# Kernel tuning notes

Measured on AMD Instinct MI355X. Metric: run time of the kernel, lower is better.

Reference implementation:

```python
import jax, jax.numpy as jnp
import numpy as np

B, DIM, H, W = 8, 128, 128, 128
QK, MLP, HEADS, NT, GS = 128, 256, 4, 8, 128


def _ln(x, w, b):
    m = jnp.mean(x, -1, keepdims=True)
    v = jnp.mean((x - m) ** 2, -1, keepdims=True)
    return (x - m) * jax.lax.rsqrt(v + 1e-5) * w + b


def _norml2(x):
    n = jnp.sqrt(jnp.sum(x * x, -1, keepdims=True))
    return x / jnp.maximum(n, 1e-12)


def setup_inputs() -> dict:
    key = jax.random.key(0)
    ks = jax.random.split(key, 12)
    s = 0.02
    f32 = jnp.float32
    return {
        'x': jax.random.normal(ks[0], (B, DIM, H, W), f32),
        'means': jax.random.normal(ks[1], (NT, DIM), f32),
        'ln1_w': jnp.ones((DIM,), f32), 'ln1_b': jnp.zeros((DIM,), f32),
        'wq': jax.random.normal(ks[2], (QK, DIM), f32) * s,
        'wk': jax.random.normal(ks[3], (QK, DIM), f32) * s,
        'wv': jax.random.normal(ks[4], (DIM, DIM), f32) * s,
        'wproj': jax.random.normal(ks[5], (DIM, DIM), f32) * s,
        'irca_wk': jax.random.normal(ks[6], (QK, DIM), f32) * s,
        'irca_wv': jax.random.normal(ks[7], (DIM, DIM), f32) * s,
        'conv1x1_w': jax.random.normal(ks[8], (DIM, DIM), f32) * s,
        'ln2_w': jnp.ones((DIM,), f32), 'ln2_b': jnp.zeros((DIM,), f32),
        'fc1_w': jax.random.normal(ks[9], (MLP, DIM), f32) * s,
        'fc1_b': jnp.zeros((MLP,), f32),
        'dw_w': jax.random.normal(ks[10], (MLP, 1, 5, 5), f32) * s,
        'dw_b': jnp.zeros((MLP,), f32),
        'fc2_w': jax.random.normal(ks[11], (DIM, MLP), f32) * s,
        'fc2_b': jnp.zeros((DIM,), f32),
    }


def reference(x, means, ln1_w, ln1_b, wq, wk, wv, wproj, irca_wk, irca_wv,
              conv1x1_w, ln2_w, ln2_b, fc1_w, fc1_b, dw_w, dw_b, fc2_w, fc2_b):
    Bx, C, Hh, Ww = x.shape
    N = Hh * Ww
    xt = x.reshape(Bx, C, N).transpose(0, 2, 1)          # b n c
    residual = xt
    xn = _ln(xt, ln1_w, ln1_b)
    m = jax.lax.stop_gradient(means)                      # eval: means buffer, detached
    # IRCA (eval path): global K/V from cluster means
    dq, dv = QK // HEADS, C // HEADS
    kg = (m @ irca_wk.T).reshape(NT, HEADS, dq).transpose(1, 0, 2)  # h nt dq
    vg = (m @ irca_wv.T).reshape(NT, HEADS, dv).transpose(1, 0, 2)  # h nt dv
    # cluster assignment -> token reordering (no grad)
    scores = jnp.einsum('bic,jc->bij', _norml2(xn), _norml2(m))
    buckets = jnp.argmax(scores, axis=-1)
    idx = jnp.argsort(buckets, axis=-1)                   # [B,N] permutation
    # IASA
    q = xn @ wq.T
    k = xn @ wk.T
    v = xn @ wv.T
    take = lambda t: jnp.take_along_axis(t, idx[:, :, None], axis=1)
    q, k, v = take(q), take(k), take(v)
    gs = min(N, GS)
    ng = (N + gs - 1) // gs
    pad_n = ng * gs - N
    qp = jnp.concatenate([q, jnp.flip(q[:, N - pad_n:N], axis=1)], axis=1)
    qp = qp.reshape(Bx, ng, gs, HEADS, dq).transpose(0, 1, 3, 2, 4)  # b g h gs dq

    def window(t, d):
        tp = jnp.concatenate([t, jnp.flip(t[:, N - pad_n - gs:N], axis=1)], axis=1)
        blk = tp.reshape(Bx, ng + 1, gs, HEADS, d)
        win = jnp.concatenate([blk[:, :-1], blk[:, 1:]], axis=2)     # b g 2gs h d
        return win.transpose(0, 1, 3, 2, 4)

    kp = window(k, dq)
    vp = window(v, dv)
    scale = 1.0 / np.sqrt(dq)
    a1 = jax.nn.softmax(jnp.einsum('bghqd,bghkd->bghqk', qp, kp) * scale, axis=-1)
    out1 = jnp.einsum('bghqk,bghkd->bghqd', a1, vp)
    a2 = jax.nn.softmax(jnp.einsum('bghqd,hkd->bghqk', qp, kg) * scale, axis=-1)
    out2 = jnp.einsum('bghqk,hkd->bghqd', a2, vg)
    out = (out1 + out2).transpose(0, 1, 3, 2, 4).reshape(Bx, ng * gs, C)[:, :N]
    inv = jnp.argsort(idx, axis=-1)                       # scatter-back = inverse perm
    out = jnp.take_along_axis(out, inv[:, :, None], axis=1)
    out = out @ wproj.T
    yimg = out.transpose(0, 2, 1).reshape(Bx, C, Hh, Ww)
    yimg = jnp.einsum('oc,bchw->bohw', conv1x1_w, yimg)
    x2 = residual + yimg.reshape(Bx, C, N).transpose(0, 2, 1)
    # ConvFFN with PreNorm
    xm = _ln(x2, ln2_w, ln2_b)
    h1 = jax.nn.gelu(xm @ fc1_w.T + fc1_b, approximate=False)
    himg = h1.transpose(0, 2, 1).reshape(Bx, MLP, Hh, Ww)
    dwc = jax.lax.conv_general_dilated(himg, dw_w, (1, 1), 'SAME',
                                       feature_group_count=MLP,
                                       dimension_numbers=('NCHW', 'OIHW', 'NCHW'))
    dwc = jax.nn.gelu(dwc + dw_b.reshape(1, MLP, 1, 1), approximate=False)
    h1 = h1 + dwc.reshape(Bx, MLP, N).transpose(0, 2, 1)
    x3 = x2 + (h1 @ fc2_w.T + fc2_b)
    return x3.transpose(0, 2, 1).reshape(Bx, C, Hh, Ww)
```

## Files before the change

kernel.cpp:

```cpp
#include <hip/hip_runtime.h>
#include <math.h>

typedef unsigned short u16;
typedef unsigned int u32;
typedef __attribute__((ext_vector_type(8))) short bf16x8;
typedef __attribute__((ext_vector_type(4))) float f32x4;

constexpr int BB   = 8;
constexpr int DIMC = 128;
constexpr int HH   = 128;
constexpr int WW   = 128;
constexpr int NTOK = HH * WW;
constexpr int QKD  = 128;
constexpr int MLPD = 256;
constexpr int NTm  = 8;
constexpr int GSZ  = 128;
constexpr int NGRP = NTOK / GSZ;
constexpr size_t BIG = 16777216;

__device__ __forceinline__ float gelu_f(float v) {
    return 0.5f * v * (1.0f + erff(v * 0.70710678118654752440f));
}
__device__ __forceinline__ float b2f(u16 u) {
    return __uint_as_float(((u32)u) << 16);
}
__device__ __forceinline__ u16 f2b(float f) {
    u32 x = __float_as_uint(f);
    return (u16)((x + 0x7fffu + ((x >> 16) & 1u)) >> 16);
}
__device__ __forceinline__ float ulo(u32 u) { return __uint_as_float(u << 16); }
__device__ __forceinline__ float uhi(u32 u) { return __uint_as_float(u & 0xffff0000u); }

__global__ __launch_bounds__(128) void k_prep(const float* __restrict__ means,
        const float* __restrict__ iwk, const float* __restrict__ iwv,
        float* __restrict__ mhat, u16* __restrict__ kgbb, u16* __restrict__ vgtb) {
    __shared__ float sm[DIMC];
    __shared__ float inv_s;
    int tt = blockIdx.x;
    int t = threadIdx.x;
    sm[t] = means[tt * DIMC + t];
    __syncthreads();
    if (t == 0) {
        float s = 0.f;
        for (int c = 0; c < DIMC; c++) s += sm[c] * sm[c];
        inv_s = 1.f / fmaxf(sqrtf(s), 1e-12f);
    }
    __syncthreads();
    mhat[tt * DIMC + t] = sm[t] * inv_s;
    float sk = 0.f, sv = 0.f;
    #pragma unroll 8
    for (int c = 0; c < DIMC; c++) {
        sk = fmaf(sm[c], iwk[t * DIMC + c], sk);
        sv = fmaf(sm[c], iwv[t * DIMC + c], sv);
    }
    kgbb[tt * DIMC + t] = f2b(sk);
    vgtb[(t >> 5) * 256 + (t & 31) * 8 + tt] = f2b(sv);
}

__global__ __launch_bounds__(256) void k_cvtall(const float* __restrict__ wq,
        const float* __restrict__ wk, const float* __restrict__ wv,
        const float* __restrict__ fc1, const float* __restrict__ fc2,
        u16* __restrict__ wqkv, u16* __restrict__ fc1b, u16* __restrict__ fc2b) {
    int i = blockIdx.x * 256 + threadIdx.x;
    if (i < 49152) {
        const float* s = (i < 16384) ? wq : (i < 32768 ? wk : wv);
        wqkv[i] = f2b(s[i & 16383]);
    } else if (i < 81920) {
        fc1b[i - 49152] = f2b(fc1[i - 49152]);
    } else if (i < 114688) {
        fc2b[i - 81920] = f2b(fc2[i - 81920]);
    }
}

__global__ __launch_bounds__(256) void k_fuse(const float* __restrict__ c1,
        const float* __restrict__ wp, u16* __restrict__ wf) {
    __shared__ float wpS[DIMC * DIMC];
    int t = threadIdx.x;
    for (int i = t; i < DIMC * DIMC; i += 256) wpS[i] = wp[i];
    __syncthreads();
    int o = blockIdx.x * 2 + (t >> 7);
    int c = t & 127;
    float s = 0.f;
    #pragma unroll 8
    for (int m = 0; m < DIMC; m++) s = fmaf(c1[o * DIMC + m], wpS[m * DIMC + c], s);
    wf[o * DIMC + c] = f2b(s);
}

__global__ __launch_bounds__(64) void k_ln1(const float* __restrict__ x,
        const float* __restrict__ lw, const float* __restrict__ lb,
        const float* __restrict__ mhat, u16* __restrict__ xn, int* __restrict__ bucket) {
    __shared__ float smh[NTm * DIMC];
    int chunk = blockIdx.x;
    int b = chunk >> 8;
    int n = ((chunk & 255) << 6) + threadIdx.x;
    for (int i = threadIdx.x; i < NTm * DIMC; i += 64) smh[i] = mhat[i];
    __syncthreads();
    const float* xb = x + (size_t)b * DIMC * NTOK + n;
    float xv[DIMC];
    float sum = 0.f, sq = 0.f;
    #pragma unroll
    for (int c = 0; c < DIMC; c++) {
        float v = xb[(size_t)c * NTOK];
        xv[c] = v;
        sum += v; sq += v * v;
    }
    float mean = sum * (1.0f / DIMC);
    float var = sq * (1.0f / DIMC) - mean * mean;
    float rstd = rsqrtf(var + 1e-5f);
    float sc[NTm];
    #pragma unroll
    for (int j = 0; j < NTm; j++) sc[j] = 0.f;
    u16* xnr = xn + ((size_t)b * NTOK + n) * DIMC;
    #pragma unroll
    for (int c = 0; c < DIMC; c++) {
        float v = (xv[c] - mean) * rstd * lw[c] + lb[c];
        xnr[c] = f2b(v);
        #pragma unroll
        for (int j = 0; j < NTm; j++) sc[j] = fmaf(v, smh[j * DIMC + c], sc[j]);
    }
    int best = 0; float bv = sc[0];
    #pragma unroll
    for (int j = 1; j < NTm; j++) if (sc[j] > bv) { bv = sc[j]; best = j; }
    bucket[b * NTOK + n] = best;
}

__global__ __launch_bounds__(64) void k_count(const int* __restrict__ bucket, int* __restrict__ cnt) {
    int chunk = blockIdx.x;
    int bk = bucket[(chunk << 6) + threadIdx.x];
    #pragma unroll
    for (int j = 0; j < NTm; j++) {
        unsigned long long m = __ballot(bk == j);
        if (threadIdx.x == 0) cnt[chunk * NTm + j] = (int)__popcll(m);
    }
}

__global__ __launch_bounds__(64) void k_scan(const int* __restrict__ cnt, int* __restrict__ base) {
    __shared__ int sc[256 * NTm];
    __shared__ int bb[NTm], tot[NTm];
    int b = blockIdx.x, t = threadIdx.x;
    for (int i = t; i < 256 * NTm; i += 64) sc[i] = cnt[b * 256 * NTm + i];
    __syncthreads();
    if (t < NTm) {
        int run = 0;
        for (int c = 0; c < 256; c++) {
            int v = sc[c * NTm + t];
            sc[c * NTm + t] = run;
            run += v;
        }
        tot[t] = run;
    }
    __syncthreads();
    if (t == 0) {
        int a = 0;
        for (int j = 0; j < NTm; j++) { bb[j] = a; a += tot[j]; }
    }
    __syncthreads();
    for (int i = t; i < 256 * NTm; i += 64) base[b * 256 * NTm + i] = sc[i] + bb[i & 7];
}

__global__ __launch_bounds__(64) void k_place(const int* __restrict__ bucket,
        const int* __restrict__ base, int* __restrict__ gidx) {
    int chunk = blockIdx.x;
    int lane = threadIdx.x;
    int nf = (chunk << 6) + lane;
    int bk = bucket[nf];
    unsigned long long lower = (1ull << lane) - 1ull;
    int rank = 0;
    #pragma unroll
    for (int j = 0; j < NTm; j++) {
        unsigned long long m = __ballot(bk == j);
        if (bk == j) rank = (int)__popcll(m & lower);
    }
    int b = nf >> 14;
    int pos = base[chunk * NTm + bk] + rank;
    gidx[b * NTOK + pos] = nf & (NTOK - 1);
}

__global__ __launch_bounds__(256) void k_inv(const int* __restrict__ gidx, u16* __restrict__ iinv) {
    int i = blockIdx.x * 256 + threadIdx.x;
    int b = i >> 14;
    iinv[((size_t)b << 14) + gidx[i]] = (u16)(i & (NTOK - 1));
}

template<int KDIM, int NOUT, int GATHER, int AIMG, int BIASF, int GELUF, int RES, int STIMG, int CBF, int LN2F>
__global__ __launch_bounds__(256) void g_mfma(const u16* __restrict__ A, const u16* __restrict__ W,
        const float* __restrict__ bias, const void* __restrict__ resid,
        const int* __restrict__ gidx, void* __restrict__ Cout, float ascale,
        const float* __restrict__ lnw, const float* __restrict__ lnb, void* __restrict__ Cout2) {
    __shared__ u16 As[128 * 40];
    __shared__ u16 Ws[128 * 40];
    const int b = blockIdx.z;
    const int m0 = blockIdx.x * 128;
    const int n0 = blockIdx.y * 128;
    const int t = threadIdx.x;
    const int lane = t & 63;
    const int wave = t >> 6;
    const int wm = (wave & 1) * 64;
    const int wn = (wave >> 1) * 64;
    const int srow = t >> 2;
    const int sko = (t & 3) * 8;
    const u16* pA0 = nullptr; const u16* pA1 = nullptr;
    if (!AIMG) {
        int ra0 = m0 + srow, ra1 = m0 + 64 + srow;
        if (GATHER == 1) {
            ra0 = gidx[b * NTOK + ra0];
            ra1 = gidx[b * NTOK + ra1];
        } else if (GATHER == 2) {
            const u16* gi = (const u16*)gidx;
            ra0 = gi[b * NTOK + ra0];
            ra1 = gi[b * NTOK + ra1];
        }
        pA0 = A + ((size_t)b * NTOK + ra0) * KDIM + sko;
        pA1 = A + ((size_t)b * NTOK + ra1) * KDIM + sko;
    }
    const u16* pW0 = W + (size_t)(n0 + srow) * KDIM + sko;
    const u16* pW1 = W + (size_t)(n0 + 64 + srow) * KDIM + sko;

    f32x4 acc[4][4];
    #pragma unroll
    for (int i = 0; i < 4; i++)
        #pragma unroll
        for (int j = 0; j < 4; j++) acc[i][j] = (f32x4){0.f, 0.f, 0.f, 0.f};

    for (int k0 = 0; k0 < KDIM; k0 += 32) {
        uint4 a0, a1, w0, w1;
        u16 e[16];
        if (!AIMG) {
            a0 = *(const uint4*)(pA0 + k0);
            a1 = *(const uint4*)(pA1 + k0);
        } else {
            const int kk2 = t & 31;
            const int tg = t >> 5;
            const u16* src = A + ((size_t)b * KDIM + k0 + kk2) * NTOK + m0 + tg * 16;
            *(uint4*)&e[0] = *(const uint4*)src;
            *(uint4*)&e[8] = *(const uint4*)(src + 8);
        }
        w0 = *(const uint4*)(pW0 + k0);
        w1 = *(const uint4*)(pW1 + k0);
        __syncthreads();
        if (!AIMG) {
            *(uint4*)&As[srow * 40 + sko] = a0;
            *(uint4*)&As[(64 + srow) * 40 + sko] = a1;
        } else {
            const int kk2 = t & 31;
            const int tg = t >> 5;
            #pragma unroll
            for (int j = 0; j < 16; j++) As[(tg * 16 + j) * 40 + kk2] = e[j];
        }
        *(uint4*)&Ws[srow * 40 + sko] = w0;
        *(uint4*)&Ws[(64 + srow) * 40 + sko] = w1;
        __syncthreads();
        bf16x8 af[4], bfv[4];
        #pragma unroll
        for (int i = 0; i < 4; i++)
            af[i] = *(bf16x8*)&As[(wm + i * 16 + (lane & 15)) * 40 + (lane >> 4) * 8];
        #pragma unroll
        for (int j = 0; j < 4; j++)
            bfv[j] = *(bf16x8*)&Ws[(wn + j * 16 + (lane & 15)) * 40 + (lane >> 4) * 8];
        #pragma unroll
        for (int i = 0; i < 4; i++)
            #pragma unroll
            for (int j = 0; j < 4; j++)
                acc[i][j] = __builtin_amdgcn_mfma_f32_16x16x32_bf16(af[i], bfv[j], acc[i][j], 0, 0, 0);
    }

    const int c2 = lane & 15, gq2 = lane >> 4;
    int colj[4];
    #pragma unroll
    for (int j = 0; j < 4; j++) colj[j] = n0 + wn + j * 16 + c2;

    if (LN2F) {
        #pragma unroll
        for (int i = 0; i < 4; i++) {
            int rbase = m0 + wm + i * 16 + gq2 * 4;
            #pragma unroll
            for (int j = 0; j < 4; j++) {
                const float* rf = (const float*)resid;
                float4 rr = *(const float4*)&rf[((size_t)b * NOUT + colj[j]) * NTOK + rbase];
                acc[i][j][0] += rr.x; acc[i][j][1] += rr.y;
                acc[i][j][2] += rr.z; acc[i][j][3] += rr.w;
            }
        }
        __syncthreads();
        float* ps = (float*)&As[0];
        const int h = wn >> 6;
        float mean_[4][4], rstd_[4][4];
        #pragma unroll
        for (int i = 0; i < 4; i++)
            #pragma unroll
            for (int r = 0; r < 4; r++) {
                float s = 0.f, q = 0.f;
                #pragma unroll
                for (int j = 0; j < 4; j++) { float tv = acc[i][j][r]; s += tv; q += tv * tv; }
                s += __shfl_xor(s, 1, 64); q += __shfl_xor(q, 1, 64);
                s += __shfl_xor(s, 2, 64); q += __shfl_xor(q, 2, 64);
                s += __shfl_xor(s, 4, 64); q += __shfl_xor(q, 4, 64);
                s += __shfl_xor(s, 8, 64); q += __shfl_xor(q, 8, 64);
                if (c2 == 0) {
                    int rl = wm + i * 16 + gq2 * 4 + r;
                    ps[(h * 128 + rl) * 2 + 0] = s;
                    ps[(h * 128 + rl) * 2 + 1] = q;
                }
            }
        __syncthreads();
        #pragma unroll
        for (int i = 0; i < 4; i++)
            #pragma unroll
            for (int r = 0; r < 4; r++) {
                int rl = wm + i * 16 + gq2 * 4 + r;
                float s = ps[rl * 2 + 0] + ps[(128 + rl) * 2 + 0];
                float q = ps[rl * 2 + 1] + ps[(128 + rl) * 2 + 1];
                float mn = s * (1.0f / 128.0f);
                float vr = q * (1.0f / 128.0f) - mn * mn;
                mean_[i][r] = mn;
                rstd_[i][r] = rsqrtf(vr + 1e-5f);
            }
        float lwj[4], lbj[4];
        #pragma unroll
        for (int j = 0; j < 4; j++) { lwj[j] = lnw[colj[j]]; lbj[j] = lnb[colj[j]]; }
        u16* xo = (u16*)Cout;
        u16* mo = (u16*)Cout2;
        #pragma unroll
        for (int i = 0; i < 4; i++) {
            int rbase = m0 + wm + i * 16 + gq2 * 4;
            #pragma unroll
            for (int j = 0; j < 4; j++)
                #pragma unroll
                for (int r = 0; r < 4; r++) {
                    float tv = acc[i][j][r];
                    size_t off = ((size_t)b * NTOK + rbase + r) * NOUT + colj[j];
                    xo[off] = f2b(tv);
                    mo[off] = f2b((tv - mean_[i][r]) * rstd_[i][r] * lwj[j] + lbj[j]);
                }
        }
        return;
    }

    const float smul = (blockIdx.y == 0) ? ascale : 1.0f;
    float bj[4];
    #pragma unroll
    for (int j = 0; j < 4; j++) bj[j] = BIASF ? bias[colj[j]] : 0.f;
    #pragma unroll
    for (int i = 0; i < 4; i++) {
        int rbase = m0 + wm + i * 16 + gq2 * 4;
        #pragma unroll
        for (int j = 0; j < 4; j++) {
            f32x4 v = acc[i][j];
            v[0] *= smul; v[1] *= smul; v[2] *= smul; v[3] *= smul;
            if (BIASF) { v[0] += bj[j]; v[1] += bj[j]; v[2] += bj[j]; v[3] += bj[j]; }
            if (GELUF) { v[0] = gelu_f(v[0]); v[1] = gelu_f(v[1]); v[2] = gelu_f(v[2]); v[3] = gelu_f(v[3]); }
            if (RES == 1) {
                const float* rf = (const float*)resid;
                float4 rr = *(const float4*)&rf[((size_t)b * NOUT + colj[j]) * NTOK + rbase];
                v[0] += rr.x; v[1] += rr.y; v[2] += rr.z; v[3] += rr.w;
            } else if (RES == 3) {
                const u16* rb = (const u16*)resid;
                #pragma unroll
                for (int r = 0; r < 4; r++)
                    v[r] += b2f(rb[((size_t)b * NTOK + rbase + r) * NOUT + colj[j]]);
            }
            if (STIMG) {
                size_t off = ((size_t)b * NOUT + colj[j]) * NTOK + rbase;
                if (CBF) {
                    ushort4 o;
                    o.x = f2b(v[0]); o.y = f2b(v[1]); o.z = f2b(v[2]); o.w = f2b(v[3]);
                    *(ushort4*)((u16*)Cout + off) = o;
                } else {
                    *(float4*)((float*)Cout + off) = make_float4(v[0], v[1], v[2], v[3]);
                }
            } else {
                if (CBF) {
                    #pragma unroll
                    for (int r = 0; r < 4; r++)
                        ((u16*)Cout)[((size_t)b * NTOK + rbase + r) * NOUT + colj[j]] = f2b(v[r]);
                } else {
                    #pragma unroll
                    for (int r = 0; r < 4; r++)
                        ((float*)Cout)[((size_t)b * NTOK + rbase + r) * NOUT + colj[j]] = v[r];
                }
            }
        }
    }
}

__global__ __launch_bounds__(256, 3) void k_attn(const u16* __restrict__ qkv,
        const u16* __restrict__ kgbb, const u16* __restrict__ vgtb,
        u16* __restrict__ outp) {
    __shared__ u16 VT[2][32][264];
    __shared__ u16 Pb[4][64][40];
    const int g = blockIdx.x, hp = blockIdx.y, b = blockIdx.z;
    const int t = threadIdx.x;
    const int wave = t >> 6, lane = t & 63;
    const int c = lane & 15, gq = lane >> 4;
    const int lh = wave & 1, head = hp * 2 + lh, qh = wave >> 1;
    const size_t brow = (size_t)b * NTOK;

    {
        int key = t;
        int pos = (key < GSZ) ? g * GSZ + key
                : (g == NGRP - 1 ? NTOK - 1 - (key - GSZ) : g * GSZ + key);
        const u16* vp = qkv + (brow + pos) * 384 + 256 + hp * 64;
        #pragma unroll
        for (int i = 0; i < 8; i++) {
            uint4 v = *(const uint4*)(vp + i * 8);
            u16 e[8];
            *(uint4*)e = v;
            #pragma unroll
            for (int j = 0; j < 8; j++) {
                int d = i * 8 + j;
                VT[d >> 5][d & 31][key] = e[j];
            }
        }
        if (t < 64) {
            int l2 = t >> 5, dv = t & 31;
            uint4 v = *(const uint4*)(vgtb + ((size_t)(hp * 2 + l2) * 32 + dv) * 8);
            *(uint4*)&VT[l2][dv][256] = v;
        }
    }

    const int q0 = g * GSZ + qh * 64;
    bf16x8 qf[4];
    #pragma unroll
    for (int nq = 0; nq < 4; nq++)
        qf[nq] = *(const bf16x8*)(qkv + (brow + q0 + nq * 16 + c) * 384 + head * 32 + gq * 8);

    const u16* kbp = qkv + brow * 384 + 128 + head * 32 + gq * 8;
    bf16x8 kfa[8][2];
    #pragma unroll
    for (int s = 0; s < 8; s++)
        #pragma unroll
        for (int mk = 0; mk < 2; mk++) {
            int kl = s * 32 + mk * 16 + c;
            int pos = (kl < GSZ) ? g * GSZ + kl
                    : (g == NGRP - 1 ? NTOK - 1 - (kl - GSZ) : g * GSZ + kl);
            kfa[s][mk] = *(const bf16x8*)(kbp + (size_t)pos * 384);
        }
    bf16x8 kgf = *(const bf16x8*)(kgbb + (c & 7) * 128 + head * 32 + gq * 8);

    __syncthreads();

    f32x4 acc[4][2];
    #pragma unroll
    for (int i = 0; i < 4; i++)
        #pragma unroll
        for (int j = 0; j < 2; j++) acc[i][j] = (f32x4){0.f, 0.f, 0.f, 0.f};
    float lsum[4] = {0.f, 0.f, 0.f, 0.f};

    for (int s = 0; s < 8; s++) {
        #pragma unroll
        for (int mk = 0; mk < 2; mk++) {
            #pragma unroll
            for (int nq = 0; nq < 4; nq++) {
                f32x4 st = __builtin_amdgcn_mfma_f32_16x16x32_bf16(kfa[s][mk], qf[nq],
                        (f32x4){0.f, 0.f, 0.f, 0.f}, 0, 0, 0);
                float p0 = __expf(st[0]), p1 = __expf(st[1]);
                float p2 = __expf(st[2]), p3 = __expf(st[3]);
                lsum[nq] += (p0 + p1) + (p2 + p3);
                u32 r0, r1;
                asm("v_cvt_pk_bf16_f32 %0, %1, %2" : "=v"(r0) : "v"(p0), "v"(p1));
                asm("v_cvt_pk_bf16_f32 %0, %1, %2" : "=v"(r1) : "v"(p2), "v"(p3));
                *(uint2*)&Pb[wave][nq * 16 + c][mk * 16 + gq * 4] = make_uint2(r0, r1);
            }
        }
        __builtin_amdgcn_sched_barrier(0);
        bf16x8 pf[4], vf[2];
        #pragma unroll
        for (int mt = 0; mt < 4; mt++)
            pf[mt] = *(const bf16x8*)&Pb[wave][mt * 16 + c][gq * 8];
        #pragma unroll
        for (int nv = 0; nv < 2; nv++)
            vf[nv] = *(const bf16x8*)&VT[lh][nv * 16 + c][s * 32 + gq * 8];
        #pragma unroll
        for (int mt = 0; mt < 4; mt++)
            #pragma unroll
            for (int nv = 0; nv < 2; nv++)
                acc[mt][nv] = __builtin_amdgcn_mfma_f32_16x16x32_bf16(pf[mt], vf[nv], acc[mt][nv], 0, 0, 0);
    }

    #pragma unroll
    for (int nq = 0; nq < 4; nq++) {
        lsum[nq] += __shfl_xor(lsum[nq], 16, 64);
        lsum[nq] += __shfl_xor(lsum[nq], 32, 64);
    }

    {
        #pragma unroll
        for (int nq = 0; nq < 4; nq++) {
            f32x4 sg = __builtin_amdgcn_mfma_f32_16x16x32_bf16(kgf, qf[nq],
                    (f32x4){0.f, 0.f, 0.f, 0.f}, 0, 0, 0);
            float p0, p1, p2, p3;
            if (gq < 2) {
                p0 = __expf(sg[0]); p1 = __expf(sg[1]);
                p2 = __expf(sg[2]); p3 = __expf(sg[3]);
            } else { p0 = p1 = p2 = p3 = 0.f; }
            float lg = (p0 + p1) + (p2 + p3);
            lg += __shfl_xor(lg, 16, 64);
            lg += __shfl_xor(lg, 32, 64);
            float w = lsum[nq] / lg;
            p0 *= w; p1 *= w; p2 *= w; p3 *= w;
            u32 r0, r1;
            asm("v_cvt_pk_bf16_f32 %0, %1, %2" : "=v"(r0) : "v"(p0), "v"(p1));
            asm("v_cvt_pk_bf16_f32 %0, %1, %2" : "=v"(r1) : "v"(p2), "v"(p3));
            *(uint2*)&Pb[wave][nq * 16 + c][gq * 4] = make_uint2(r0, r1);
        }
        __builtin_amdgcn_sched_barrier(0);
        bf16x8 zf;
        #pragma unroll
        for (int z8 = 0; z8 < 8; z8++) zf[z8] = 0;
        bf16x8 pf[4], vf[2];
        #pragma unroll
        for (int mt = 0; mt < 4; mt++)
            pf[mt] = *(const bf16x8*)&Pb[wave][mt * 16 + c][gq * 8];
        #pragma unroll
        for (int nv = 0; nv < 2; nv++)
            vf[nv] = (gq == 0) ? *(const bf16x8*)&VT[lh][nv * 16 + c][256] : zf;
        #pragma unroll
        for (int mt = 0; mt < 4; mt++)
            #pragma unroll
            for (int nv = 0; nv < 2; nv++)
                acc[mt][nv] = __builtin_amdgcn_mfma_f32_16x16x32_bf16(pf[mt], vf[nv], acc[mt][nv], 0, 0, 0);
    }

    float* lf = (float*)&Pb[wave][0][0];
    if (gq == 0) {
        #pragma unroll
        for (int nq = 0; nq < 4; nq++) lf[nq * 16 + c] = lsum[nq];
    }
    __builtin_amdgcn_sched_barrier(0);
    u16 ov[4][2][4];
    #pragma unroll
    for (int mt = 0; mt < 4; mt++) {
        float il[4];
        #pragma unroll
        for (int r = 0; r < 4; r++)
            il[r] = 1.f / lf[mt * 16 + gq * 4 + r];
        #pragma unroll
        for (int nv = 0; nv < 2; nv++)
            #pragma unroll
            for (int r = 0; r < 4; r++)
                ov[mt][nv][r] = f2b(acc[mt][nv][r] * il[r]);
    }

    __syncthreads();
    u16* st = (u16*)&VT[0][0][0];
    #pragma unroll
    for (int mt = 0; mt < 4; mt++)
        #pragma unroll
        for (int nv = 0; nv < 2; nv++)
            #pragma unroll
            for (int r = 0; r < 4; r++)
                st[(qh * 64 + mt * 16 + gq * 4 + r) * 68 + lh * 32 + nv * 16 + c] = ov[mt][nv][r];
    __syncthreads();
    {
        const int rl0 = t >> 3;
        const int seg = t & 7;
        #pragma unroll
        for (int p = 0; p < 4; p++) {
            int rl = rl0 + p * 32;
            uint4 v4 = *(const uint4*)&st[rl * 68 + seg * 8];
            *(uint4*)&outp[(brow + g * GSZ + rl) * 128 + hp * 64 + seg * 8] = v4;
        }
    }
}

__global__ __launch_bounds__(256) void k_dw(const u16* __restrict__ himg,
        const float* __restrict__ dww, const float* __restrict__ dwb, u16* __restrict__ dsum) {
    const int mc = blockIdx.y, b = blockIdx.z;
    const int t = threadIdx.x;
    const int y = blockIdx.x * 32 + (t >> 4) * 2;
    const int xb = (t & 15) * 8;
    float wgt[25];
    #pragma unroll
    for (int i = 0; i < 25; i++) wgt[i] = dww[mc * 25 + i];
    const float bsv = dwb[mc];
    const u16* src = himg + ((size_t)b * MLPD + mc) * NTOK;
    u16* dst = dsum + ((size_t)b * MLPD + mc) * NTOK;

    float w[6][12];
    #pragma unroll
    for (int r = 0; r < 6; r++) {
        int ysrc = y - 2 + r;
        bool vy = (ysrc >= 0 && ysrc < HH);
        const u16* rp = src + ysrc * WW + xb;
        uint4 aq = vy ? *(const uint4*)(rp - 8) : make_uint4(0u, 0u, 0u, 0u);
        uint4 bq = vy ? *(const uint4*)(rp)     : make_uint4(0u, 0u, 0u, 0u);
        uint4 cq = vy ? *(const uint4*)(rp + 8) : make_uint4(0u, 0u, 0u, 0u);
        w[r][0]  = ulo(aq.w); w[r][1]  = uhi(aq.w);
        w[r][2]  = ulo(bq.x); w[r][3]  = uhi(bq.x);
        w[r][4]  = ulo(bq.y); w[r][5]  = uhi(bq.y);
        w[r][6]  = ulo(bq.z); w[r][7]  = uhi(bq.z);
        w[r][8]  = ulo(bq.w); w[r][9]  = uhi(bq.w);
        w[r][10] = ulo(cq.x); w[r][11] = uhi(cq.x);
        if (xb == 0)   { w[r][0]  = 0.f; w[r][1]  = 0.f; }
        if (xb == 120) { w[r][10] = 0.f; w[r][11] = 0.f; }
    }

    float acc0[8], acc1[8];
    #pragma unroll
    for (int px = 0; px < 8; px++) { acc0[px] = 0.f; acc1[px] = 0.f; }
    #pragma unroll
    for (int dy = 0; dy < 5; dy++)
        #pragma unroll
        for (int dx = 0; dx < 5; dx++) {
            float wv = wgt[dy * 5 + dx];
            #pragma unroll
            for (int px = 0; px < 8; px++) {
                acc0[px] = fmaf(wv, w[dy][px + dx], acc0[px]);
                acc1[px] = fmaf(wv, w[dy + 1][px + dx], acc1[px]);
            }
        }

    u32 o0[4], o1[4];
    #pragma unroll
    for (int px = 0; px < 8; px += 2) {
        u16 a0 = f2b(w[2][px + 2] + gelu_f(acc0[px] + bsv));
        u16 a1 = f2b(w[2][px + 3] + gelu_f(acc0[px + 1] + bsv));
        o0[px >> 1] = (u32)a0 | ((u32)a1 << 16);
        u16 b0 = f2b(w[3][px + 2] + gelu_f(acc1[px] + bsv));
        u16 b1 = f2b(w[3][px + 3] + gelu_f(acc1[px + 1] + bsv));
        o1[px >> 1] = (u32)b0 | ((u32)b1 << 16);
    }
    *(uint4*)(dst + y * WW + xb) = *(uint4*)o0;
    *(uint4*)(dst + (y + 1) * WW + xb) = *(uint4*)o1;
}

extern "C" void kernel_launch(void* const* d_in, const int* in_sizes, int n_in,
                              void* d_out, int out_size, void* d_ws, size_t ws_size,
                              hipStream_t stream) {
    const float* x       = (const float*)d_in[0];
    const float* means   = (const float*)d_in[1];
    const float* ln1_w   = (const float*)d_in[2];
    const float* ln1_b   = (const float*)d_in[3];
    const float* wq      = (const float*)d_in[4];
    const float* wk      = (const float*)d_in[5];
    const float* wv      = (const float*)d_in[6];
    const float* wproj   = (const float*)d_in[7];
    const float* irca_wk = (const float*)d_in[8];
    const float* irca_wv = (const float*)d_in[9];
    const float* conv1w  = (const float*)d_in[10];
    const float* ln2_w   = (const float*)d_in[11];
    const float* ln2_b   = (const float*)d_in[12];
    const float* fc1_w   = (const float*)d_in[13];
    const float* fc1_b   = (const float*)d_in[14];
    const float* dw_w    = (const float*)d_in[15];
    const float* dw_b    = (const float*)d_in[16];
    const float* fc2_w   = (const float*)d_in[17];
    const float* fc2_b   = (const float*)d_in[18];
    float* out = (float*)d_out;

    const size_t need = 202514432;
    if (ws_size < need) return;

    char* base = (char*)d_ws;
    float* mhat  = (float*)(base);
    u16*   kgbb  = (u16*)(base + 4096);
    u16*   vgtb  = (u16*)(base + 6144);
    int*   bucket = (int*)(base + 8192);
    u16*   wqkv  = (u16*)(base + 8192);
    u16*   wfub  = wqkv + 3 * 16384;
    u16*   fc1b  = wfub + 16384;
    u16*   fc2b  = fc1b + 32768;
    u16*   iinv  = (u16*)(base + 270336);
    int*   cnt   = (int*)(base + 532480);
    int*   cbase = (int*)(base + 598016);
    int*   gidx  = (int*)(base + 663552);
    u16*   Abase = (u16*)(base + 1187840);
    u16*   x2b   = (u16*)(base + 101851136);
    u16*   dsum  = (u16*)(base + 135405568);

    u16* qkv  = Abase;
    u16* himg = Abase;
    u16* xmb  = Abase + 2 * BIG;
    u16* xnb   = (u16*)d_out;
    u16* attnb = (u16*)d_out;

    k_prep<<<NTm, 128, 0, stream>>>(means, irca_wk, irca_wv, mhat, kgbb, vgtb);
    k_ln1<<<BB * NTOK / 64, 64, 0, stream>>>(x, ln1_w, ln1_b, mhat, xnb, bucket);
    k_count<<<BB * NTOK / 64, 64, 0, stream>>>(bucket, cnt);
    k_scan<<<BB, 64, 0, stream>>>(cnt, cbase);
    k_place<<<BB * NTOK / 64, 64, 0, stream>>>(bucket, cbase, gidx);
    k_inv<<<BB * NTOK / 256, 256, 0, stream>>>(gidx, iinv);

    k_cvtall<<<448, 256, 0, stream>>>(wq, wk, wv, fc1_w, fc2_w, wqkv, fc1b, fc2b);
    k_fuse<<<64, 256, 0, stream>>>(conv1w, wproj, wfub);

    const float qsc = 0.17677669529663687f;
    g_mfma<128, 384, 1, 0, 0, 0, 0, 0, 1, 0><<<dim3(128, 3, BB), 256, 0, stream>>>(
        xnb, wqkv, nullptr, nullptr, gidx, qkv, qsc, nullptr, nullptr, nullptr);

    k_attn<<<dim3(NGRP, 2, BB), 256, 0, stream>>>(qkv, kgbb, vgtb, attnb);

    g_mfma<128, 128, 2, 0, 0, 0, 1, 0, 1, 1><<<dim3(128, 1, BB), 256, 0, stream>>>(
        attnb, wfub, nullptr, x, (const int*)iinv, x2b, 1.0f, ln2_w, ln2_b, xmb);

    g_mfma<128, 256, 0, 0, 1, 1, 0, 1, 1, 0><<<dim3(128, 2, BB), 256, 0, stream>>>(
        xmb, fc1b, fc1_b, nullptr, nullptr, himg, 1.0f, nullptr, nullptr, nullptr);
    k_dw<<<dim3(4, MLPD, BB), 256, 0, stream>>>(himg, dw_w, dw_b, dsum);
    g_mfma<256, 128, 0, 1, 1, 0, 3, 1, 0, 0><<<dim3(128, 1, BB), 256, 0, stream>>>(
        dsum, fc2b, fc2_b, x2b, nullptr, out, 1.0f, nullptr, nullptr, nullptr);

    (void)in_sizes; (void)n_in; (void)out_size;
}
```

Measured before the change: 342.7 us.

## Split LN1 channels across four waves with shared-memory reduction

```diff
diff --git a/kernel.cpp b/kernel.cpp
--- a/kernel.cpp
+++ b/kernel.cpp
@@ -86,42 +86,82 @@
     wf[o * DIMC + c] = f2b(s);
 }
 
-__global__ __launch_bounds__(64) void k_ln1(const float* __restrict__ x,
+__global__ __launch_bounds__(256) void k_ln1(const float* __restrict__ x,
         const float* __restrict__ lw, const float* __restrict__ lb,
         const float* __restrict__ mhat, u16* __restrict__ xn, int* __restrict__ bucket) {
     __shared__ float smh[NTm * DIMC];
-    int chunk = blockIdx.x;
-    int b = chunk >> 8;
-    int n = ((chunk & 255) << 6) + threadIdx.x;
-    for (int i = threadIdx.x; i < NTm * DIMC; i += 64) smh[i] = mhat[i];
-    __syncthreads();
-    const float* xb = x + (size_t)b * DIMC * NTOK + n;
-    float xv[DIMC];
+    __shared__ float lwb[DIMC], lbb[DIMC];
+    __shared__ float red[4][64][3];
+    __shared__ float scr[4][64][9];
+    const int chunk = blockIdx.x;
+    const int b = chunk >> 8;
+    const int n0 = (chunk & 255) << 6;
+    const int t = threadIdx.x;
+    const int cg = t >> 6, tok = t & 63;
+    const int n = n0 + tok;
+    const int cbase = cg * 32;
+    for (int i = t; i < NTm * DIMC; i += 256) smh[i] = mhat[i];
+    if (t < DIMC) { lwb[t] = lw[t]; lbb[t] = lb[t]; }
+
+    const float* xb = x + (size_t)b * DIMC * NTOK + (size_t)cbase * NTOK + n;
+    float xv[32];
     float sum = 0.f, sq = 0.f;
     #pragma unroll
-    for (int c = 0; c < DIMC; c++) {
+    for (int c = 0; c < 32; c++) {
         float v = xb[(size_t)c * NTOK];
         xv[c] = v;
         sum += v; sq += v * v;
     }
-    float mean = sum * (1.0f / DIMC);
-    float var = sq * (1.0f / DIMC) - mean * mean;
+    red[cg][tok][0] = sum;
+    red[cg][tok][1] = sq;
+    __syncthreads();
+    float s0 = red[0][tok][0] + red[1][tok][0] + red[2][tok][0] + red[3][tok][0];
+    float q0 = red[0][tok][1] + red[1][tok][1] + red[2][tok][1] + red[3][tok][1];
+    float mean = s0 * (1.0f / DIMC);
+    float var = q0 * (1.0f / DIMC) - mean * mean;
     float rstd = rsqrtf(var + 1e-5f);
+
     float sc[NTm];
     #pragma unroll
     for (int j = 0; j < NTm; j++) sc[j] = 0.f;
-    u16* xnr = xn + ((size_t)b * NTOK + n) * DIMC;
-    #pragma unroll
-    for (int c = 0; c < DIMC; c++) {
-        float v = (xv[c] - mean) * rstd * lw[c] + lb[c];
-        xnr[c] = f2b(v);
-        #pragma unroll
-        for (int j = 0; j < NTm; j++) sc[j] = fmaf(v, smh[j * DIMC + c], sc[j]);
-    }
-    int best = 0; float bv = sc[0];
-    #pragma unroll
-    for (int j = 1; j < NTm; j++) if (sc[j] > bv) { bv = sc[j]; best = j; }
-    bucket[b * NTOK + n] = best;
+    u32 opk[16];
+    #pragma unroll
+    for (int c = 0; c < 32; c += 2) {
+        float v0 = (xv[c]     - mean) * rstd * lwb[cbase + c]     + lbb[cbase + c];
+        float v1 = (xv[c + 1] - mean) * rstd * lwb[cbase + c + 1] + lbb[cbase + c + 1];
+        #pragma unroll
+        for (int j = 0; j < NTm; j++) {
+            sc[j] = fmaf(v0, smh[j * DIMC + cbase + c], sc[j]);
+            sc[j] = fmaf(v1, smh[j * DIMC + cbase + c + 1], sc[j]);
+        }
+        opk[c >> 1] = (u32)f2b(v0) | ((u32)f2b(v1) << 16);
+    }
+    u16* xnr = xn + ((size_t)b * NTOK + n) * DIMC + cbase;
+    *(uint4*)(xnr + 0)  = make_uint4(opk[0],  opk[1],  opk[2],  opk[3]);
+    *(uint4*)(xnr + 8)  = make_uint4(opk[4],  opk[5],  opk[6],  opk[7]);
+    *(uint4*)(xnr + 16) = make_uint4(opk[8],  opk[9],  opk[10], opk[11]);
+    *(uint4*)(xnr + 24) = make_uint4(opk[12], opk[13], opk[14], opk[15]);
+
+    #pragma unroll
+    for (int j = 0; j < NTm; j++) scr[cg][tok][j] = sc[j];
+    __syncthreads();
+    if (cg == 0) {
+        int best = 0; float bv = 0.f;
+        #pragma unroll
+        for (int j = 0; j < NTm; j++) {
+            float v = ((scr[0][tok][j] + scr[1][tok][j]) +
+                       (scr[2][tok][j] + scr[3][tok][j]));
+            if (j == 0 || v > bv) { bv = v; best = (v > bv || j == 0) ? ((j == 0) ? 0 : j) : best; }
+        }
+        float v0 = ((scr[0][tok][0] + scr[1][tok][0]) + (scr[2][tok][0] + scr[3][tok][0]));
+        best = 0; bv = v0;
+        #pragma unroll
+        for (int j = 1; j < NTm; j++) {
+            float v = ((scr[0][tok][j] + scr[1][tok][j]) + (scr[2][tok][j] + scr[3][tok][j]));
+            if (v > bv) { bv = v; best = j; }
+        }
+        bucket[b * NTOK + n] = best;
+    }
 }
 
 __global__ __launch_bounds__(64) void k_count(const int* __restrict__ bucket, int* __restrict__ cnt) {
@@ -675,7 +715,7 @@
     u16* attnb = (u16*)d_out;
 
     k_prep<<<NTm, 128, 0, stream>>>(means, irca_wk, irca_wv, mhat, kgbb, vgtb);
-    k_ln1<<<BB * NTOK / 64, 64, 0, stream>>>(x, ln1_w, ln1_b, mhat, xnb, bucket);
+    k_ln1<<<BB * NTOK / 64, 256, 0, stream>>>(x, ln1_w, ln1_b, mhat, xnb, bucket);
     k_count<<<BB * NTOK / 64, 64, 0, stream>>>(bucket, cnt);
     k_scan<<<BB, 64, 0, stream>>>(cnt, cbase);
     k_place<<<BB * NTOK / 64, 64, 0, stream>>>(bucket, cbase, gidx);
```

Result: faster. 321.9 us (-6.1%).
